# Kernel optimization log

Measured on AMD Instinct MI355X. Metric: run time of the kernel, lower is better.

## Reference

```python
import jax, jax.numpy as jnp
import numpy as np

N = 50000          # nodes
E = 800000         # directed edges (before self-loops)
F_IN = 256
HIDS = 32
HEADS = 8
N_CLASSES = 40
NEG_SLOPE = 0.2    # PyG GATConv default leaky_relu slope


def setup_inputs() -> dict:
    key = jax.random.key(0)
    ks = jax.random.split(key, 10)
    x = jax.random.normal(ks[0], (N, F_IN), dtype=jnp.float32)
    edge_index = jax.random.randint(ks[1], (2, E), 0, N, dtype=jnp.int32)
    # conv1: F_IN -> HIDS per head, HEADS heads, concat=True
    W1 = jax.random.normal(ks[2], (F_IN, HEADS * HIDS), dtype=jnp.float32) * (1.0 / np.sqrt(F_IN))
    a1_src = jax.random.normal(ks[3], (HEADS, HIDS), dtype=jnp.float32) * 0.1
    a1_dst = jax.random.normal(ks[4], (HEADS, HIDS), dtype=jnp.float32) * 0.1
    b1 = jnp.zeros((HEADS * HIDS,), dtype=jnp.float32)
    # conv2: HEADS*HIDS -> N_CLASSES, 1 head, concat=False
    W2 = jax.random.normal(ks[5], (HEADS * HIDS, N_CLASSES), dtype=jnp.float32) * (1.0 / np.sqrt(HEADS * HIDS))
    a2_src = jax.random.normal(ks[6], (1, N_CLASSES), dtype=jnp.float32) * 0.1
    a2_dst = jax.random.normal(ks[7], (1, N_CLASSES), dtype=jnp.float32) * 0.1
    b2 = jnp.zeros((N_CLASSES,), dtype=jnp.float32)
    return {"x": x, "edge_index": edge_index, "W1": W1, "a1_src": a1_src,
            "a1_dst": a1_dst, "b1": b1, "W2": W2, "a2_src": a2_src,
            "a2_dst": a2_dst, "b2": b2}


def _gat_conv(x, src, dst, W, a_src, a_dst, bias, heads, concat):
    n = x.shape[0]
    c = W.shape[1] // heads
    xw = (x @ W).reshape(n, heads, c)                       # [N,H,C]
    alpha_s = jnp.einsum('nhc,hc->nh', xw, a_src)           # [N,H]
    alpha_d = jnp.einsum('nhc,hc->nh', xw, a_dst)
    e = alpha_s[src] + alpha_d[dst]                         # [Etot,H]
    e = jnp.where(e >= 0, e, NEG_SLOPE * e)                 # leaky_relu
    # segment softmax over incoming edges of each destination node
    m = jax.ops.segment_max(e, dst, num_segments=n)         # [N,H]
    ex = jnp.exp(e - m[dst])
    denom = jax.ops.segment_sum(ex, dst, num_segments=n)    # [N,H]
    alpha = ex / denom[dst]                                 # [Etot,H]
    out = jax.ops.segment_sum(alpha[:, :, None] * xw[src], dst, num_segments=n)  # [N,H,C]
    if concat:
        out = out.reshape(n, heads * c)
    else:
        out = out.mean(axis=1)
    return out + bias


def reference(x, edge_index, W1, a1_src, a1_dst, b1, W2, a2_src, a2_dst, b2):
    n = x.shape[0]
    # add self-loops (PyG GATConv default)
    loop = jnp.arange(n, dtype=edge_index.dtype)
    src = jnp.concatenate([edge_index[0], loop])
    dst = jnp.concatenate([edge_index[1], loop])
    # dropout(p=0.6) layers are identity in eval mode
    h = _gat_conv(x, src, dst, W1, a1_src, a1_dst, b1, HEADS, True)
    h = jax.nn.elu(h)
    out = _gat_conv(h, src, dst, W2, a2_src, a2_dst, b2, 1, False)
    return out
```

## Files before the change

### kernel.cpp

```cpp
#include <hip/hip_runtime.h>
#include <hip/hip_bf16.h>

#define NNODES 50000
#define NPAD   50048
#define NEDGES 800000
#define ETOT   (NEDGES + NNODES)
#define FIN    256
#define HIDS   32
#define HEADS  8
#define NCLS   40
#define NEG    0.2f

#define SCAN_B 256
#define NSCB   ((NNODES + SCAN_B - 1) / SCAN_B)

#define PB_X    (NPAD * 32 / 256)
#define PB_W1   256
#define PB_W2   64
#define PB_CNT  ((NNODES + 255) / 256)
#define PB_HPAD ((NPAD - NNODES))

typedef __attribute__((ext_vector_type(8))) short bf16x8;
typedef __attribute__((ext_vector_type(4))) float f32x4;

__device__ __forceinline__ ushort f2bf(float f) {
  unsigned u = __float_as_uint(f);
  unsigned r = (u + 0x7fffu + ((u >> 16) & 1u)) >> 16;
  return (ushort)r;
}
__device__ __forceinline__ float bf2f(ushort u) {
  return __uint_as_float(((unsigned)u) << 16);
}

__global__ __launch_bounds__(256) void prep_k(
    const float* __restrict__ x, const float* __restrict__ W1, const float* __restrict__ W2,
    ushort* __restrict__ xb, ushort* __restrict__ w1t, ushort* __restrict__ w2t,
    int* __restrict__ cnt, ushort* __restrict__ hb) {
  int b = blockIdx.x, t = threadIdx.x;
  if (b < PB_X) {
    size_t gid = (size_t)b * 256 + t;
    int row = (int)(gid >> 5);
    int c0 = ((int)gid & 31) * 8;
    bf16x8 o;
    if (row < NNODES) {
      const float4* xp = (const float4*)(x + (size_t)row * 256 + c0);
      float4 a = xp[0], bb = xp[1];
      o[0] = (short)f2bf(a.x); o[1] = (short)f2bf(a.y);
      o[2] = (short)f2bf(a.z); o[3] = (short)f2bf(a.w);
      o[4] = (short)f2bf(bb.x); o[5] = (short)f2bf(bb.y);
      o[6] = (short)f2bf(bb.z); o[7] = (short)f2bf(bb.w);
    } else {
      o = (bf16x8)0;
    }
    *(bf16x8*)(xb + (size_t)row * 256 + c0) = o;
  } else if (b < PB_X + PB_W1) {
    int idx = (b - PB_X) * 256 + t;
    int k = idx >> 8, n = idx & 255;
    w1t[(size_t)n * 256 + k] = f2bf(W1[(size_t)k * 256 + n]);
  } else if (b < PB_X + PB_W1 + PB_W2) {
    int idx = (b - PB_X - PB_W1) * 256 + t;
    int n = idx >> 8, k = idx & 255;
    w2t[(size_t)n * 256 + k] = (n < NCLS) ? f2bf(W2[(size_t)k * NCLS + n]) : (ushort)0;
  } else if (b < PB_X + PB_W1 + PB_W2 + PB_CNT) {
    int i = (b - PB_X - PB_W1 - PB_W2) * 256 + t;
    if (i < NNODES) cnt[i] = 0;
  } else {
    int idx = (b - PB_X - PB_W1 - PB_W2 - PB_CNT);
    int row = NNODES + idx;
    hb[(size_t)row * 256 + t] = 0;
  }
}

__global__ __launch_bounds__(256) void gemm1_mfma(
    const ushort* __restrict__ xb, const ushort* __restrict__ w1t, ushort* __restrict__ xw1b) {
  __shared__ ushort As[64 * 40];
  __shared__ ushort Bs[256 * 40];
  const int tid = threadIdx.x;
  const int m0 = blockIdx.x * 64;
  const int w = tid >> 6, l = tid & 63, lr = l & 15, lq = l >> 4;
  f32x4 acc[4][4];
#pragma unroll
  for (int i = 0; i < 4; ++i)
#pragma unroll
    for (int j = 0; j < 4; ++j) acc[i][j] = (f32x4)0.f;

  for (int k0 = 0; k0 < 256; k0 += 32) {
    {
      int row = tid >> 2, kg = (tid & 3) * 8;
      *(bf16x8*)&As[row * 40 + kg] = *(const bf16x8*)(xb + (size_t)(m0 + row) * 256 + k0 + kg);
    }
#pragma unroll
    for (int p = 0; p < 4; ++p) {
      int idx = tid + p * 256;
      int n = idx >> 2, kg = (idx & 3) * 8;
      *(bf16x8*)&Bs[n * 40 + kg] = *(const bf16x8*)(w1t + (size_t)n * 256 + k0 + kg);
    }
    __syncthreads();
    bf16x8 af[4], bf[4];
#pragma unroll
    for (int mt = 0; mt < 4; ++mt)
      af[mt] = *(const bf16x8*)&As[(mt * 16 + lr) * 40 + lq * 8];
#pragma unroll
    for (int nt = 0; nt < 4; ++nt)
      bf[nt] = *(const bf16x8*)&Bs[((w * 4 + nt) * 16 + lr) * 40 + lq * 8];
#pragma unroll
    for (int mt = 0; mt < 4; ++mt)
#pragma unroll
      for (int nt = 0; nt < 4; ++nt)
        acc[mt][nt] = __builtin_amdgcn_mfma_f32_16x16x32_bf16(af[mt], bf[nt], acc[mt][nt], 0, 0, 0);
    __syncthreads();
  }
#pragma unroll
  for (int mt = 0; mt < 4; ++mt)
#pragma unroll
    for (int nt = 0; nt < 4; ++nt)
#pragma unroll
      for (int r = 0; r < 4; ++r) {
        int row = m0 + mt * 16 + lq * 4 + r;
        int col = (w * 4 + nt) * 16 + lr;
        xw1b[(size_t)row * 256 + col] = f2bf(acc[mt][nt][r]);
      }
}

__global__ __launch_bounds__(256) void gemm2_mfma(
    const ushort* __restrict__ hb, const ushort* __restrict__ w2t, ushort* __restrict__ xw2b) {
  const int tid = threadIdx.x;
  const int w = tid >> 6, l = tid & 63, lr = l & 15, lq = l >> 4;
  const int row0 = blockIdx.x * 64 + w * 16;
  f32x4 acc[4];
#pragma unroll
  for (int i = 0; i < 4; ++i) acc[i] = (f32x4)0.f;
#pragma unroll
  for (int ks = 0; ks < 8; ++ks) {
    int k0 = ks * 32;
    bf16x8 af = *(const bf16x8*)(hb + (size_t)(row0 + lr) * 256 + k0 + lq * 8);
#pragma unroll
    for (int nt = 0; nt < 4; ++nt) {
      bf16x8 bfr = *(const bf16x8*)(w2t + (size_t)(nt * 16 + lr) * 256 + k0 + lq * 8);
      acc[nt] = __builtin_amdgcn_mfma_f32_16x16x32_bf16(af, bfr, acc[nt], 0, 0, 0);
    }
  }
#pragma unroll
  for (int nt = 0; nt < 4; ++nt) {
    int col = nt * 16 + lr;
    if (col < NCLS) {
#pragma unroll
      for (int r = 0; r < 4; ++r) {
        int row = row0 + lq * 4 + r;
        xw2b[(size_t)row * 40 + col] = f2bf(acc[nt][r]);
      }
    }
  }
}

__global__ __launch_bounds__(256) void alpha1_k(
    const ushort* __restrict__ xw1b, const float* __restrict__ a1src,
    const float* __restrict__ a1dst, float* __restrict__ os, float* __restrict__ od, int n) {
  int wid = (blockIdx.x * 256 + threadIdx.x) >> 6;
  if (wid >= n) return;
  int lane = threadIdx.x & 63;
  ushort4 u = *(const ushort4*)(xw1b + (size_t)wid * 256 + lane * 4);
  float4 xv = make_float4(bf2f(u.x), bf2f(u.y), bf2f(u.z), bf2f(u.w));
  float4 as = *reinterpret_cast<const float4*>(a1src + lane * 4);
  float4 ad = *reinterpret_cast<const float4*>(a1dst + lane * 4);
  float s = xv.x * as.x + xv.y * as.y + xv.z * as.z + xv.w * as.w;
  float d = xv.x * ad.x + xv.y * ad.y + xv.z * ad.z + xv.w * ad.w;
#pragma unroll
  for (int off = 1; off < 8; off <<= 1) {
    s += __shfl_xor(s, off, 64);
    d += __shfl_xor(d, off, 64);
  }
  if ((lane & 7) == 0) {
    os[(size_t)wid * 8 + (lane >> 3)] = s;
    od[(size_t)wid * 8 + (lane >> 3)] = d;
  }
}

__global__ __launch_bounds__(256) void hist_k(const int* __restrict__ dstA, int* __restrict__ cnt) {
  int e = blockIdx.x * 256 + threadIdx.x;
  if (e >= ETOT) return;
  int d = (e < NEDGES) ? dstA[e] : (e - NEDGES);
  atomicAdd(&cnt[d], 1);
}

__global__ __launch_bounds__(SCAN_B) void scan1_k(const int* __restrict__ deg,
                                                  int* __restrict__ row_ptr,
                                                  int* __restrict__ bsum) {
  __shared__ int sm[SCAN_B];
  int b = blockIdx.x, t = threadIdx.x;
  int idx = b * SCAN_B + t;
  int v = (idx < NNODES) ? deg[idx] : 0;
  sm[t] = v;
  __syncthreads();
#pragma unroll
  for (int off = 1; off < SCAN_B; off <<= 1) {
    int u = (t >= off) ? sm[t - off] : 0;
    __syncthreads();
    sm[t] += u;
    __syncthreads();
  }
  if (idx < NNODES) row_ptr[idx + 1] = sm[t];
  if (t == SCAN_B - 1) bsum[b] = sm[t];
}

__global__ __launch_bounds__(256) void scan2_k(int* __restrict__ bsum) {
  __shared__ int sm[256];
  int t = threadIdx.x;
  sm[t] = (t < NSCB) ? bsum[t] : 0;
  __syncthreads();
#pragma unroll
  for (int off = 1; off < 256; off <<= 1) {
    int u = (t >= off) ? sm[t - off] : 0;
    __syncthreads();
    sm[t] += u;
    __syncthreads();
  }
  if (t < NSCB) bsum[t] = (t > 0) ? sm[t - 1] : 0;
}

__global__ __launch_bounds__(SCAN_B) void scan3_k(const int* __restrict__ bsum,
                                                  int* __restrict__ row_ptr) {
  int b = blockIdx.x, t = threadIdx.x;
  int idx = b * SCAN_B + t;
  if (idx < NNODES) row_ptr[idx + 1] += bsum[b];
  if (b == 0 && t == 0) row_ptr[0] = 0;
}

__global__ __launch_bounds__(256) void scatter_k(const int* __restrict__ srcA, const int* __restrict__ dstA,
                                                 const int* __restrict__ row_ptr, int* __restrict__ cnt,
                                                 int* __restrict__ col) {
  int e = blockIdx.x * 256 + threadIdx.x;
  if (e >= ETOT) return;
  int s, d;
  if (e < NEDGES) { s = srcA[e]; d = dstA[e]; }
  else { s = d = e - NEDGES; }
  int old = atomicSub(&cnt[d], 1);
  col[row_ptr[d] + old - 1] = s;
}

__global__ __launch_bounds__(256) void agg1_k(
    const ushort* __restrict__ xw1b, const float* __restrict__ a1s, const float* __restrict__ a1d,
    const int* __restrict__ row_ptr, const int* __restrict__ col,
    const float* __restrict__ b1, ushort* __restrict__ hb, int n) {
  int wid = (blockIdx.x * 256 + threadIdx.x) >> 6;
  if (wid >= n) return;
  int lane = threadIdx.x & 63;
  int hh = lane >> 3;
  int beg = row_ptr[wid], end = row_ptr[wid + 1];
  float ad = a1d[(size_t)wid * 8 + hh];
  float denom = 0.f, ax = 0.f, ay = 0.f, az = 0.f, aw = 0.f;
  int i = beg;
  for (; i + 4 <= end; i += 4) {
    int s0 = col[i], s1 = col[i + 1], s2 = col[i + 2], s3 = col[i + 3];
    float e0 = a1s[(size_t)s0 * 8 + hh] + ad;
    float e1 = a1s[(size_t)s1 * 8 + hh] + ad;
    float e2 = a1s[(size_t)s2 * 8 + hh] + ad;
    float e3 = a1s[(size_t)s3 * 8 + hh] + ad;
    ushort4 u0 = *(const ushort4*)(xw1b + (size_t)s0 * 256 + lane * 4);
    ushort4 u1 = *(const ushort4*)(xw1b + (size_t)s1 * 256 + lane * 4);
    ushort4 u2 = *(const ushort4*)(xw1b + (size_t)s2 * 256 + lane * 4);
    ushort4 u3 = *(const ushort4*)(xw1b + (size_t)s3 * 256 + lane * 4);
    float w0 = __expf(fmaxf(e0, 0.f) + NEG * fminf(e0, 0.f));
    float w1 = __expf(fmaxf(e1, 0.f) + NEG * fminf(e1, 0.f));
    float w2 = __expf(fmaxf(e2, 0.f) + NEG * fminf(e2, 0.f));
    float w3 = __expf(fmaxf(e3, 0.f) + NEG * fminf(e3, 0.f));
    denom += (w0 + w1) + (w2 + w3);
    ax += w0 * bf2f(u0.x) + w1 * bf2f(u1.x) + w2 * bf2f(u2.x) + w3 * bf2f(u3.x);
    ay += w0 * bf2f(u0.y) + w1 * bf2f(u1.y) + w2 * bf2f(u2.y) + w3 * bf2f(u3.y);
    az += w0 * bf2f(u0.z) + w1 * bf2f(u1.z) + w2 * bf2f(u2.z) + w3 * bf2f(u3.z);
    aw += w0 * bf2f(u0.w) + w1 * bf2f(u1.w) + w2 * bf2f(u2.w) + w3 * bf2f(u3.w);
  }
  for (; i < end; ++i) {
    int s = col[i];
    float e = a1s[(size_t)s * 8 + hh] + ad;
    float w = __expf(fmaxf(e, 0.f) + NEG * fminf(e, 0.f));
    ushort4 u = *(const ushort4*)(xw1b + (size_t)s * 256 + lane * 4);
    denom += w;
    ax += w * bf2f(u.x); ay += w * bf2f(u.y); az += w * bf2f(u.z); aw += w * bf2f(u.w);
  }
  float inv = 1.f / denom;
  float4 bv = *reinterpret_cast<const float4*>(b1 + lane * 4);
  float ox = ax * inv + bv.x;
  float oy = ay * inv + bv.y;
  float oz = az * inv + bv.z;
  float ow = aw * inv + bv.w;
  ox = (ox > 0.f) ? ox : expm1f(ox);
  oy = (oy > 0.f) ? oy : expm1f(oy);
  oz = (oz > 0.f) ? oz : expm1f(oz);
  ow = (ow > 0.f) ? ow : expm1f(ow);
  ushort4 ho;
  ho.x = f2bf(ox); ho.y = f2bf(oy); ho.z = f2bf(oz); ho.w = f2bf(ow);
  *(ushort4*)(hb + (size_t)wid * 256 + lane * 4) = ho;
}

__global__ __launch_bounds__(256) void alpha2_k(
    const ushort* __restrict__ xw2b, const float* __restrict__ a2s_in, const float* __restrict__ a2d_in,
    float* __restrict__ os, float* __restrict__ od, int n) {
  int v = blockIdx.x * 256 + threadIdx.x;
  if (v >= n) return;
  const ushort* row = xw2b + (size_t)v * 40;
  float s = 0.f, d = 0.f;
#pragma unroll
  for (int j = 0; j < 10; ++j) {
    ushort4 u = *(const ushort4*)(row + j * 4);
    float4 as = *reinterpret_cast<const float4*>(a2s_in + j * 4);
    float4 ad = *reinterpret_cast<const float4*>(a2d_in + j * 4);
    s += bf2f(u.x) * as.x + bf2f(u.y) * as.y + bf2f(u.z) * as.z + bf2f(u.w) * as.w;
    d += bf2f(u.x) * ad.x + bf2f(u.y) * ad.y + bf2f(u.z) * ad.z + bf2f(u.w) * ad.w;
  }
  os[v] = s;
  od[v] = d;
}

__global__ __launch_bounds__(256) void agg2_k(
    const ushort* __restrict__ xw2b, const float* __restrict__ a2s, const float* __restrict__ a2d,
    const int* __restrict__ row_ptr, const int* __restrict__ col,
    const float* __restrict__ b2, float* __restrict__ out, int n) {
  int wid = (blockIdx.x * 256 + threadIdx.x) >> 6;
  if (wid >= n) return;
  int lane = threadIdx.x & 63;
  int beg = row_ptr[wid], end = row_ptr[wid + 1];
  float ad = a2d[wid];
  float denom = 0.f, acc = 0.f;
  int i = beg;
  for (; i + 4 <= end; i += 4) {
    int s0 = col[i], s1 = col[i + 1], s2 = col[i + 2], s3 = col[i + 3];
    float e0 = a2s[s0] + ad;
    float e1 = a2s[s1] + ad;
    float e2 = a2s[s2] + ad;
    float e3 = a2s[s3] + ad;
    float w0 = __expf(fmaxf(e0, 0.f) + NEG * fminf(e0, 0.f));
    float w1 = __expf(fmaxf(e1, 0.f) + NEG * fminf(e1, 0.f));
    float w2 = __expf(fmaxf(e2, 0.f) + NEG * fminf(e2, 0.f));
    float w3 = __expf(fmaxf(e3, 0.f) + NEG * fminf(e3, 0.f));
    float x0 = 0.f, x1 = 0.f, x2 = 0.f, x3 = 0.f;
    if (lane < NCLS) {
      x0 = bf2f(xw2b[(size_t)s0 * 40 + lane]);
      x1 = bf2f(xw2b[(size_t)s1 * 40 + lane]);
      x2 = bf2f(xw2b[(size_t)s2 * 40 + lane]);
      x3 = bf2f(xw2b[(size_t)s3 * 40 + lane]);
    }
    denom += (w0 + w1) + (w2 + w3);
    acc += w0 * x0 + w1 * x1 + w2 * x2 + w3 * x3;
  }
  for (; i < end; ++i) {
    int s = col[i];
    float e = a2s[s] + ad;
    float w = __expf(fmaxf(e, 0.f) + NEG * fminf(e, 0.f));
    denom += w;
    if (lane < NCLS) acc += w * bf2f(xw2b[(size_t)s * 40 + lane]);
  }
  if (lane < NCLS) out[(size_t)wid * 40 + lane] = acc / denom + b2[lane];
}

extern "C" void kernel_launch(void* const* d_in, const int* in_sizes, int n_in,
                              void* d_out, int out_size, void* d_ws, size_t ws_size,
                              hipStream_t stream) {
  const float* x     = (const float*)d_in[0];
  const int*   ei    = (const int*)d_in[1];
  const float* W1    = (const float*)d_in[2];
  const float* a1src = (const float*)d_in[3];
  const float* a1dst = (const float*)d_in[4];
  const float* b1    = (const float*)d_in[5];
  const float* W2    = (const float*)d_in[6];
  const float* a2src = (const float*)d_in[7];
  const float* a2dst = (const float*)d_in[8];
  const float* b2    = (const float*)d_in[9];
  float* out = (float*)d_out;

  const int* srcA = ei;
  const int* dstA = ei + NEDGES;

  ushort* xb   = (ushort*)d_ws;
  ushort* w1t  = xb + (size_t)NPAD * 256;
  ushort* w2t  = w1t + 65536;
  ushort* xw1b = w2t + 16384;
  ushort* hb   = xw1b + (size_t)NPAD * 256;
  ushort* xw2b = hb + (size_t)NPAD * 256;
  float* a1s   = (float*)(xw2b + (size_t)NPAD * 40);
  float* a1d   = a1s + (size_t)NNODES * 8;
  float* a2s   = a1d + (size_t)NNODES * 8;
  float* a2d   = a2s + NNODES;
  int* row_ptr = (int*)(a2d + NNODES);
  int* cnt     = row_ptr + (NNODES + 1);
  int* col     = cnt + NNODES;
  int* bsum    = col + ETOT;

  prep_k<<<PB_X + PB_W1 + PB_W2 + PB_CNT + PB_HPAD, 256, 0, stream>>>(
      x, W1, W2, xb, w1t, w2t, cnt, hb);

  gemm1_mfma<<<NPAD / 64, 256, 0, stream>>>(xb, w1t, xw1b);

  alpha1_k<<<(NNODES + 3) / 4, 256, 0, stream>>>(xw1b, a1src, a1dst, a1s, a1d, NNODES);

  hist_k<<<(ETOT + 255) / 256, 256, 0, stream>>>(dstA, cnt);
  scan1_k<<<NSCB, SCAN_B, 0, stream>>>(cnt, row_ptr, bsum);
  scan2_k<<<1, 256, 0, stream>>>(bsum);
  scan3_k<<<NSCB, SCAN_B, 0, stream>>>(bsum, row_ptr);
  scatter_k<<<(ETOT + 255) / 256, 256, 0, stream>>>(srcA, dstA, row_ptr, cnt, col);

  agg1_k<<<(NNODES + 3) / 4, 256, 0, stream>>>(xw1b, a1s, a1d, row_ptr, col, b1, hb, NNODES);

  gemm2_mfma<<<NPAD / 64, 256, 0, stream>>>(hb, w2t, xw2b);

  alpha2_k<<<(NNODES + 255) / 256, 256, 0, stream>>>(xw2b, a2src, a2dst, a2s, a2d, NNODES);

  agg2_k<<<(NNODES + 3) / 4, 256, 0, stream>>>(xw2b, a2s, a2d, row_ptr, col, b2, out, NNODES);
}
```

Measured before the change: 267.4 us.

## Fold attention projections into GEMMs, fuse x conversion, split aggregation across two waves

Precomputes W·a_src and W·a_dst as extra weight columns, so the attention logits come out of the GEMMs directly. This removes the separate alpha1 and alpha2 kernels. The fp32→bf16 conversion of x moves into the GEMM1 A-tile load, which drops the xb staging buffer and its extra pass over memory. The aggregation kernels now split each node's edge list across two waves and combine the partial sums through shared memory, giving more parallelism per node. In exchange, GEMM1 does 25% more MFMA work, the logits are computed from bf16 inputs (a small accuracy change), and the aggregation kernels add a block barrier.

```diff
diff --git a/kernel.cpp b/kernel.cpp
--- a/kernel.cpp
+++ b/kernel.cpp
@@ -14,12 +14,6 @@
 #define SCAN_B 256
 #define NSCB   ((NNODES + SCAN_B - 1) / SCAN_B)
 
-#define PB_X    (NPAD * 32 / 256)
-#define PB_W1   256
-#define PB_W2   64
-#define PB_CNT  ((NNODES + 255) / 256)
-#define PB_HPAD ((NPAD - NNODES))
-
 typedef __attribute__((ext_vector_type(8))) short bf16x8;
 typedef __attribute__((ext_vector_type(4))) float f32x4;
 
@@ -33,146 +27,161 @@
 }
 
 __global__ __launch_bounds__(256) void prep_k(
-    const float* __restrict__ x, const float* __restrict__ W1, const float* __restrict__ W2,
-    ushort* __restrict__ xb, ushort* __restrict__ w1t, ushort* __restrict__ w2t,
+    const float* __restrict__ W1, const float* __restrict__ W2,
+    const float* __restrict__ a1src, const float* __restrict__ a1dst,
+    const float* __restrict__ a2src, const float* __restrict__ a2dst,
+    ushort* __restrict__ w1t, ushort* __restrict__ w2t,
     int* __restrict__ cnt, ushort* __restrict__ hb) {
   int b = blockIdx.x, t = threadIdx.x;
-  if (b < PB_X) {
-    size_t gid = (size_t)b * 256 + t;
-    int row = (int)(gid >> 5);
-    int c0 = ((int)gid & 31) * 8;
-    bf16x8 o;
-    if (row < NNODES) {
-      const float4* xp = (const float4*)(x + (size_t)row * 256 + c0);
-      float4 a = xp[0], bb = xp[1];
-      o[0] = (short)f2bf(a.x); o[1] = (short)f2bf(a.y);
-      o[2] = (short)f2bf(a.z); o[3] = (short)f2bf(a.w);
-      o[4] = (short)f2bf(bb.x); o[5] = (short)f2bf(bb.y);
-      o[6] = (short)f2bf(bb.z); o[7] = (short)f2bf(bb.w);
+  if (b < 256) {
+    int k = b, n = t;
+    w1t[(size_t)n * 256 + k] = f2bf(W1[(size_t)k * 256 + n]);
+  } else if (b < 272) {
+    int j = b - 256, k = t;
+    const float* av = (j < 8) ? (a1src + j * 32) : (a1dst + (j - 8) * 32);
+    int nb = (j < 8) ? j * 32 : (j - 8) * 32;
+    float s = 0.f;
+#pragma unroll
+    for (int c = 0; c < 32; ++c) s += W1[(size_t)k * 256 + nb + c] * av[c];
+    w1t[(size_t)(256 + j) * 256 + k] = f2bf(s);
+  } else if (b < 320) {
+    w1t[(size_t)b * 256 + t] = 0;
+  } else if (b < 384) {
+    int n = b - 320, k = t;
+    ushort v;
+    if (n < NCLS) {
+      v = f2bf(W2[(size_t)k * NCLS + n]);
+    } else if (n == 40) {
+      float s = 0.f;
+#pragma unroll
+      for (int c = 0; c < NCLS; ++c) s += W2[(size_t)k * NCLS + c] * a2src[c];
+      v = f2bf(s);
+    } else if (n == 41) {
+      float s = 0.f;
+#pragma unroll
+      for (int c = 0; c < NCLS; ++c) s += W2[(size_t)k * NCLS + c] * a2dst[c];
+      v = f2bf(s);
     } else {
-      o = (bf16x8)0;
-    }
-    *(bf16x8*)(xb + (size_t)row * 256 + c0) = o;
-  } else if (b < PB_X + PB_W1) {
-    int idx = (b - PB_X) * 256 + t;
-    int k = idx >> 8, n = idx & 255;
-    w1t[(size_t)n * 256 + k] = f2bf(W1[(size_t)k * 256 + n]);
-  } else if (b < PB_X + PB_W1 + PB_W2) {
-    int idx = (b - PB_X - PB_W1) * 256 + t;
-    int n = idx >> 8, k = idx & 255;
-    w2t[(size_t)n * 256 + k] = (n < NCLS) ? f2bf(W2[(size_t)k * NCLS + n]) : (ushort)0;
-  } else if (b < PB_X + PB_W1 + PB_W2 + PB_CNT) {
-    int i = (b - PB_X - PB_W1 - PB_W2) * 256 + t;
+      v = 0;
+    }
+    w2t[(size_t)n * 256 + k] = v;
+  } else if (b < 580) {
+    int i = (b - 384) * 256 + t;
     if (i < NNODES) cnt[i] = 0;
   } else {
-    int idx = (b - PB_X - PB_W1 - PB_W2 - PB_CNT);
-    int row = NNODES + idx;
-    hb[(size_t)row * 256 + t] = 0;
+    int r = NNODES + (b - 580);
+    hb[(size_t)r * 256 + t] = 0;
   }
 }
 
 __global__ __launch_bounds__(256) void gemm1_mfma(
-    const ushort* __restrict__ xb, const ushort* __restrict__ w1t, ushort* __restrict__ xw1b) {
+    const float* __restrict__ x, const ushort* __restrict__ w1t,
+    ushort* __restrict__ xw1b, float* __restrict__ a1s, float* __restrict__ a1d) {
   __shared__ ushort As[64 * 40];
-  __shared__ ushort Bs[256 * 40];
+  __shared__ ushort Bs[320 * 40];
   const int tid = threadIdx.x;
   const int m0 = blockIdx.x * 64;
   const int w = tid >> 6, l = tid & 63, lr = l & 15, lq = l >> 4;
-  f32x4 acc[4][4];
+  f32x4 acc[4][5];
 #pragma unroll
   for (int i = 0; i < 4; ++i)
 #pragma unroll
-    for (int j = 0; j < 4; ++j) acc[i][j] = (f32x4)0.f;
+    for (int j = 0; j < 5; ++j) acc[i][j] = (f32x4)0.f;
 
   for (int k0 = 0; k0 < 256; k0 += 32) {
     {
       int row = tid >> 2, kg = (tid & 3) * 8;
-      *(bf16x8*)&As[row * 40 + kg] = *(const bf16x8*)(xb + (size_t)(m0 + row) * 256 + k0 + kg);
-    }
-#pragma unroll
-    for (int p = 0; p < 4; ++p) {
+      int gr = m0 + row;
+      bf16x8 av;
+      if (gr < NNODES) {
+        const float4* xp = (const float4*)(x + (size_t)gr * 256 + k0 + kg);
+        float4 p0 = xp[0], p1 = xp[1];
+        av[0] = (short)f2bf(p0.x); av[1] = (short)f2bf(p0.y);
+        av[2] = (short)f2bf(p0.z); av[3] = (short)f2bf(p0.w);
+        av[4] = (short)f2bf(p1.x); av[5] = (short)f2bf(p1.y);
+        av[6] = (short)f2bf(p1.z); av[7] = (short)f2bf(p1.w);
+      } else {
+        av = (bf16x8)0;
+      }
+      *(bf16x8*)&As[row * 40 + kg] = av;
+    }
+#pragma unroll
+    for (int p = 0; p < 5; ++p) {
       int idx = tid + p * 256;
       int n = idx >> 2, kg = (idx & 3) * 8;
       *(bf16x8*)&Bs[n * 40 + kg] = *(const bf16x8*)(w1t + (size_t)n * 256 + k0 + kg);
     }
     __syncthreads();
-    bf16x8 af[4], bf[4];
+    bf16x8 af[4], bfr[5];
 #pragma unroll
     for (int mt = 0; mt < 4; ++mt)
       af[mt] = *(const bf16x8*)&As[(mt * 16 + lr) * 40 + lq * 8];
 #pragma unroll
-    for (int nt = 0; nt < 4; ++nt)
-      bf[nt] = *(const bf16x8*)&Bs[((w * 4 + nt) * 16 + lr) * 40 + lq * 8];
+    for (int nt = 0; nt < 5; ++nt) {
+      int tile = nt * 4 + w;
+      bfr[nt] = *(const bf16x8*)&Bs[(tile * 16 + lr) * 40 + lq * 8];
+    }
 #pragma unroll
     for (int mt = 0; mt < 4; ++mt)
 #pragma unroll
-      for (int nt = 0; nt < 4; ++nt)
-        acc[mt][nt] = __builtin_amdgcn_mfma_f32_16x16x32_bf16(af[mt], bf[nt], acc[mt][nt], 0, 0, 0);
+      for (int nt = 0; nt < 5; ++nt)
+        acc[mt][nt] = __builtin_amdgcn_mfma_f32_16x16x32_bf16(af[mt], bfr[nt], acc[mt][nt], 0, 0, 0);
     __syncthreads();
   }
 #pragma unroll
   for (int mt = 0; mt < 4; ++mt)
 #pragma unroll
-    for (int nt = 0; nt < 4; ++nt)
-#pragma unroll
-      for (int r = 0; r < 4; ++r) {
-        int row = m0 + mt * 16 + lq * 4 + r;
-        int col = (w * 4 + nt) * 16 + lr;
-        xw1b[(size_t)row * 256 + col] = f2bf(acc[mt][nt][r]);
+    for (int nt = 0; nt < 5; ++nt) {
+      int tile = nt * 4 + w;
+      if (tile < 16) {
+        int colc = tile * 16 + lr;
+#pragma unroll
+        for (int r = 0; r < 4; ++r) {
+          int row = m0 + mt * 16 + lq * 4 + r;
+          xw1b[(size_t)row * 256 + colc] = f2bf(acc[mt][nt][r]);
+        }
+      } else if (tile == 16) {
+#pragma unroll
+        for (int r = 0; r < 4; ++r) {
+          int row = m0 + mt * 16 + lq * 4 + r;
+          if (row < NNODES) {
+            if (lr < 8) a1s[(size_t)row * 8 + lr] = acc[mt][nt][r];
+            else        a1d[(size_t)row * 8 + lr - 8] = acc[mt][nt][r];
+          }
+        }
       }
+    }
 }
 
 __global__ __launch_bounds__(256) void gemm2_mfma(
-    const ushort* __restrict__ hb, const ushort* __restrict__ w2t, ushort* __restrict__ xw2b) {
+    const ushort* __restrict__ hb, const ushort* __restrict__ w2t,
+    ushort* __restrict__ xw2b, float* __restrict__ a2s, float* __restrict__ a2d) {
   const int tid = threadIdx.x;
   const int w = tid >> 6, l = tid & 63, lr = l & 15, lq = l >> 4;
   const int row0 = blockIdx.x * 64 + w * 16;
-  f32x4 acc[4];
-#pragma unroll
-  for (int i = 0; i < 4; ++i) acc[i] = (f32x4)0.f;
+  f32x4 acc[3];
+#pragma unroll
+  for (int i = 0; i < 3; ++i) acc[i] = (f32x4)0.f;
 #pragma unroll
   for (int ks = 0; ks < 8; ++ks) {
     int k0 = ks * 32;
     bf16x8 af = *(const bf16x8*)(hb + (size_t)(row0 + lr) * 256 + k0 + lq * 8);
 #pragma unroll
-    for (int nt = 0; nt < 4; ++nt) {
+    for (int nt = 0; nt < 3; ++nt) {
       bf16x8 bfr = *(const bf16x8*)(w2t + (size_t)(nt * 16 + lr) * 256 + k0 + lq * 8);
       acc[nt] = __builtin_amdgcn_mfma_f32_16x16x32_bf16(af, bfr, acc[nt], 0, 0, 0);
     }
   }
 #pragma unroll
-  for (int nt = 0; nt < 4; ++nt) {
-    int col = nt * 16 + lr;
-    if (col < NCLS) {
-#pragma unroll
-      for (int r = 0; r < 4; ++r) {
-        int row = row0 + lq * 4 + r;
-        xw2b[(size_t)row * 40 + col] = f2bf(acc[nt][r]);
-      }
-    }
-  }
-}
-
-__global__ __launch_bounds__(256) void alpha1_k(
-    const ushort* __restrict__ xw1b, const float* __restrict__ a1src,
-    const float* __restrict__ a1dst, float* __restrict__ os, float* __restrict__ od, int n) {
-  int wid = (blockIdx.x * 256 + threadIdx.x) >> 6;
-  if (wid >= n) return;
-  int lane = threadIdx.x & 63;
-  ushort4 u = *(const ushort4*)(xw1b + (size_t)wid * 256 + lane * 4);
-  float4 xv = make_float4(bf2f(u.x), bf2f(u.y), bf2f(u.z), bf2f(u.w));
-  float4 as = *reinterpret_cast<const float4*>(a1src + lane * 4);
-  float4 ad = *reinterpret_cast<const float4*>(a1dst + lane * 4);
-  float s = xv.x * as.x + xv.y * as.y + xv.z * as.z + xv.w * as.w;
-  float d = xv.x * ad.x + xv.y * ad.y + xv.z * ad.z + xv.w * ad.w;
-#pragma unroll
-  for (int off = 1; off < 8; off <<= 1) {
-    s += __shfl_xor(s, off, 64);
-    d += __shfl_xor(d, off, 64);
-  }
-  if ((lane & 7) == 0) {
-    os[(size_t)wid * 8 + (lane >> 3)] = s;
-    od[(size_t)wid * 8 + (lane >> 3)] = d;
+  for (int nt = 0; nt < 3; ++nt) {
+    int colc = nt * 16 + lr;
+#pragma unroll
+    for (int r = 0; r < 4; ++r) {
+      int row = row0 + lq * 4 + r;
+      if (colc < NCLS)      xw2b[(size_t)row * 40 + colc] = f2bf(acc[nt][r]);
+      else if (colc == 40)  a2s[row] = acc[nt][r];
+      else if (colc == 41)  a2d[row] = acc[nt][r];
+    }
   }
 }
 
@@ -241,16 +250,21 @@
 __global__ __launch_bounds__(256) void agg1_k(
     const ushort* __restrict__ xw1b, const float* __restrict__ a1s, const float* __restrict__ a1d,
     const int* __restrict__ row_ptr, const int* __restrict__ col,
-    const float* __restrict__ b1, ushort* __restrict__ hb, int n) {
-  int wid = (blockIdx.x * 256 + threadIdx.x) >> 6;
-  if (wid >= n) return;
-  int lane = threadIdx.x & 63;
-  int hh = lane >> 3;
-  int beg = row_ptr[wid], end = row_ptr[wid + 1];
-  float ad = a1d[(size_t)wid * 8 + hh];
+    const float* __restrict__ b1, ushort* __restrict__ hb) {
+  __shared__ float4 ps[2][64];
+  __shared__ float pd[2][64];
+  const int tid = threadIdx.x;
+  const int wave = tid >> 6, lane = tid & 63;
+  const int nl = wave >> 1, sub = wave & 1;
+  const int node = blockIdx.x * 2 + nl;
+  const int hh = lane >> 3;
+  int beg = row_ptr[node], end = row_ptr[node + 1];
+  int half = (end - beg + 1) >> 1;
+  int i = beg + sub * half;
+  int lim = sub ? end : (beg + half);
+  float ad = a1d[(size_t)node * 8 + hh];
   float denom = 0.f, ax = 0.f, ay = 0.f, az = 0.f, aw = 0.f;
-  int i = beg;
-  for (; i + 4 <= end; i += 4) {
+  for (; i + 4 <= lim; i += 4) {
     int s0 = col[i], s1 = col[i + 1], s2 = col[i + 2], s3 = col[i + 3];
     float e0 = a1s[(size_t)s0 * 8 + hh] + ad;
     float e1 = a1s[(size_t)s1 * 8 + hh] + ad;
@@ -270,7 +284,7 @@
     az += w0 * bf2f(u0.z) + w1 * bf2f(u1.z) + w2 * bf2f(u2.z) + w3 * bf2f(u3.z);
     aw += w0 * bf2f(u0.w) + w1 * bf2f(u1.w) + w2 * bf2f(u2.w) + w3 * bf2f(u3.w);
   }
-  for (; i < end; ++i) {
+  for (; i < lim; ++i) {
     int s = col[i];
     float e = a1s[(size_t)s * 8 + hh] + ad;
     float w = __expf(fmaxf(e, 0.f) + NEG * fminf(e, 0.f));
@@ -278,52 +292,48 @@
     denom += w;
     ax += w * bf2f(u.x); ay += w * bf2f(u.y); az += w * bf2f(u.z); aw += w * bf2f(u.w);
   }
-  float inv = 1.f / denom;
-  float4 bv = *reinterpret_cast<const float4*>(b1 + lane * 4);
-  float ox = ax * inv + bv.x;
-  float oy = ay * inv + bv.y;
-  float oz = az * inv + bv.z;
-  float ow = aw * inv + bv.w;
-  ox = (ox > 0.f) ? ox : expm1f(ox);
-  oy = (oy > 0.f) ? oy : expm1f(oy);
-  oz = (oz > 0.f) ? oz : expm1f(oz);
-  ow = (ow > 0.f) ? ow : expm1f(ow);
-  ushort4 ho;
-  ho.x = f2bf(ox); ho.y = f2bf(oy); ho.z = f2bf(oz); ho.w = f2bf(ow);
-  *(ushort4*)(hb + (size_t)wid * 256 + lane * 4) = ho;
-}
-
-__global__ __launch_bounds__(256) void alpha2_k(
-    const ushort* __restrict__ xw2b, const float* __restrict__ a2s_in, const float* __restrict__ a2d_in,
-    float* __restrict__ os, float* __restrict__ od, int n) {
-  int v = blockIdx.x * 256 + threadIdx.x;
-  if (v >= n) return;
-  const ushort* row = xw2b + (size_t)v * 40;
-  float s = 0.f, d = 0.f;
-#pragma unroll
-  for (int j = 0; j < 10; ++j) {
-    ushort4 u = *(const ushort4*)(row + j * 4);
-    float4 as = *reinterpret_cast<const float4*>(a2s_in + j * 4);
-    float4 ad = *reinterpret_cast<const float4*>(a2d_in + j * 4);
-    s += bf2f(u.x) * as.x + bf2f(u.y) * as.y + bf2f(u.z) * as.z + bf2f(u.w) * as.w;
-    d += bf2f(u.x) * ad.x + bf2f(u.y) * ad.y + bf2f(u.z) * ad.z + bf2f(u.w) * ad.w;
-  }
-  os[v] = s;
-  od[v] = d;
+  if (sub) {
+    ps[nl][lane] = make_float4(ax, ay, az, aw);
+    pd[nl][lane] = denom;
+  }
+  __syncthreads();
+  if (!sub) {
+    float4 o = ps[nl][lane];
+    ax += o.x; ay += o.y; az += o.z; aw += o.w;
+    denom += pd[nl][lane];
+    float inv = 1.f / denom;
+    float4 bv = *reinterpret_cast<const float4*>(b1 + lane * 4);
+    float ox = ax * inv + bv.x;
+    float oy = ay * inv + bv.y;
+    float oz = az * inv + bv.z;
+    float ow = aw * inv + bv.w;
+    ox = (ox > 0.f) ? ox : expm1f(ox);
+    oy = (oy > 0.f) ? oy : expm1f(oy);
+    oz = (oz > 0.f) ? oz : expm1f(oz);
+    ow = (ow > 0.f) ? ow : expm1f(ow);
+    ushort4 ho;
+    ho.x = f2bf(ox); ho.y = f2bf(oy); ho.z = f2bf(oz); ho.w = f2bf(ow);
+    *(ushort4*)(hb + (size_t)node * 256 + lane * 4) = ho;
+  }
 }
 
 __global__ __launch_bounds__(256) void agg2_k(
     const ushort* __restrict__ xw2b, const float* __restrict__ a2s, const float* __restrict__ a2d,
     const int* __restrict__ row_ptr, const int* __restrict__ col,
-    const float* __restrict__ b2, float* __restrict__ out, int n) {
-  int wid = (blockIdx.x * 256 + threadIdx.x) >> 6;
-  if (wid >= n) return;
-  int lane = threadIdx.x & 63;
-  int beg = row_ptr[wid], end = row_ptr[wid + 1];
-  float ad = a2d[wid];
+    const float* __restrict__ b2, float* __restrict__ out) {
+  __shared__ float ps[2][40];
+  __shared__ float pd[2];
+  const int tid = threadIdx.x;
+  const int wave = tid >> 6, lane = tid & 63;
+  const int nl = wave >> 1, sub = wave & 1;
+  const int node = blockIdx.x * 2 + nl;
+  int beg = row_ptr[node], end = row_ptr[node + 1];
+  int half = (end - beg + 1) >> 1;
+  int i = beg + sub * half;
+  int lim = sub ? end : (beg + half);
+  float ad = a2d[node];
   float denom = 0.f, acc = 0.f;
-  int i = beg;
-  for (; i + 4 <= end; i += 4) {
+  for (; i + 4 <= lim; i += 4) {
     int s0 = col[i], s1 = col[i + 1], s2 = col[i + 2], s3 = col[i + 3];
     float e0 = a2s[s0] + ad;
     float e1 = a2s[s1] + ad;
@@ -343,14 +353,25 @@
     denom += (w0 + w1) + (w2 + w3);
     acc += w0 * x0 + w1 * x1 + w2 * x2 + w3 * x3;
   }
-  for (; i < end; ++i) {
+  for (; i < lim; ++i) {
     int s = col[i];
     float e = a2s[s] + ad;
     float w = __expf(fmaxf(e, 0.f) + NEG * fminf(e, 0.f));
     denom += w;
     if (lane < NCLS) acc += w * bf2f(xw2b[(size_t)s * 40 + lane]);
   }
-  if (lane < NCLS) out[(size_t)wid * 40 + lane] = acc / denom + b2[lane];
+  if (sub) {
+    if (lane < NCLS) ps[nl][lane] = acc;
+    if (lane == 0) pd[nl] = denom;
+  }
+  __syncthreads();
+  if (!sub) {
+    denom += pd[nl];
+    if (lane < NCLS) {
+      acc += ps[nl][lane];
+      out[(size_t)node * 40 + lane] = acc / denom + b2[lane];
+    }
+  }
 }
 
 extern "C" void kernel_launch(void* const* d_in, const int* in_sizes, int n_in,
@@ -371,27 +392,23 @@
   const int* srcA = ei;
   const int* dstA = ei + NEDGES;
 
-  ushort* xb   = (ushort*)d_ws;
-  ushort* w1t  = xb + (size_t)NPAD * 256;
-  ushort* w2t  = w1t + 65536;
-  ushort* xw1b = w2t + 16384;
+  ushort* w1t  = (ushort*)d_ws;
+  ushort* w2t  = w1t + (size_t)320 * 256;
+  ushort* xw1b = w2t + (size_t)64 * 256;
   ushort* hb   = xw1b + (size_t)NPAD * 256;
   ushort* xw2b = hb + (size_t)NPAD * 256;
   float* a1s   = (float*)(xw2b + (size_t)NPAD * 40);
   float* a1d   = a1s + (size_t)NNODES * 8;
   float* a2s   = a1d + (size_t)NNODES * 8;
-  float* a2d   = a2s + NNODES;
-  int* row_ptr = (int*)(a2d + NNODES);
+  float* a2d   = a2s + NPAD;
+  int* row_ptr = (int*)(a2d + NPAD);
   int* cnt     = row_ptr + (NNODES + 1);
   int* col     = cnt + NNODES;
   int* bsum    = col + ETOT;
 
-  prep_k<<<PB_X + PB_W1 + PB_W2 + PB_CNT + PB_HPAD, 256, 0, stream>>>(
-      x, W1, W2, xb, w1t, w2t, cnt, hb);
-
-  gemm1_mfma<<<NPAD / 64, 256, 0, stream>>>(xb, w1t, xw1b);
-
-  alpha1_k<<<(NNODES + 3) / 4, 256, 0, stream>>>(xw1b, a1src, a1dst, a1s, a1d, NNODES);
+  prep_k<<<628, 256, 0, stream>>>(W1, W2, a1src, a1dst, a2src, a2dst, w1t, w2t, cnt, hb);
+
+  gemm1_mfma<<<NPAD / 64, 256, 0, stream>>>(x, w1t, xw1b, a1s, a1d);
 
   hist_k<<<(ETOT + 255) / 256, 256, 0, stream>>>(dstA, cnt);
   scan1_k<<<NSCB, SCAN_B, 0, stream>>>(cnt, row_ptr, bsum);
@@ -399,11 +416,9 @@
   scan3_k<<<NSCB, SCAN_B, 0, stream>>>(bsum, row_ptr);
   scatter_k<<<(ETOT + 255) / 256, 256, 0, stream>>>(srcA, dstA, row_ptr, cnt, col);
 
-  agg1_k<<<(NNODES + 3) / 4, 256, 0, stream>>>(xw1b, a1s, a1d, row_ptr, col, b1, hb, NNODES);
-
-  gemm2_mfma<<<NPAD / 64, 256, 0, stream>>>(hb, w2t, xw2b);
-
-  alpha2_k<<<(NNODES + 255) / 256, 256, 0, stream>>>(xw2b, a2src, a2dst, a2s, a2d, NNODES);
-
-  agg2_k<<<(NNODES + 3) / 4, 256, 0, stream>>>(xw2b, a2s, a2d, row_ptr, col, b2, out, NNODES);
-}
+  agg1_k<<<NNODES / 2, 256, 0, stream>>>(xw1b, a1s, a1d, row_ptr, col, b1, hb);
+
+  gemm2_mfma<<<NPAD / 64, 256, 0, stream>>>(hb, w2t, xw2b, a2s, a2d);
+
+  agg2_k<<<NNODES / 2, 256, 0, stream>>>(xw2b, a2s, a2d, row_ptr, col, b2, out);
+}
```

After: 266.1 us. About the same (-0.5%).
